# Kernel tuning notes

Measured on AMD Instinct MI355X. Metric: run time of the kernel, lower is better.

## Reference

```python
import jax, jax.numpy as jnp
import numpy as np

N_BINS = 10
A_CONST = 0.4
C_CONST = 500.0


def entropy(v, n=N_BINS):
    # Faithful to the torch loop: p_i = mean(v >= lo + i*s and v < lo + (i+1)*s),
    # entropy -= p*log(p) for p != 0. Vectorized over the n bins.
    v = v.reshape(-1)
    lo = v.min()
    hi = v.max()
    scale = (hi - lo) / n
    idx = jnp.arange(n, dtype=v.dtype)
    lower = lo + idx * scale                    # [n]
    upper = lower + scale                       # [n]
    mask = (v[None, :] >= lower[:, None]) & (v[None, :] < upper[:, None])  # [n, len(v)]
    p = mask.sum(axis=1).astype(v.dtype) / v.shape[0]
    safe_p = jnp.where(p > 0, p, 1.0)
    return -jnp.sum(jnp.where(p > 0, p * jnp.log(safe_p), 0.0))


def unite(p_i, p_j, w_assess, b_assess):
    # w_local = sigmoid(Linear(|p_i - p_j|)); w_global scalar from entropy gap.
    w_local = jax.nn.sigmoid(jnp.abs(p_i - p_j) @ w_assess.T + b_assess)
    w_global = A_CONST / jnp.pi * jnp.arctan(C_CONST * (entropy(p_i) - entropy(p_j))) + 0.5
    w = w_global * w_local + (1.0 - w_global)
    return p_i * w + p_j * (1.0 - w)


def setup_inputs() -> dict:
    key = jax.random.key(0)
    ks = jax.random.split(key, 11)
    B, S, H, L = 64, 512, 1024, 3
    s = 1.0 / np.sqrt(H)
    return {
        "x": jax.random.normal(ks[0], (B, S, H), jnp.float32),
        "base_dense_w": jax.random.normal(ks[1], (H, H), jnp.float32) * s,
        "base_dense_b": jax.random.normal(ks[2], (H,), jnp.float32) * s,
        "base_out_w": jax.random.normal(ks[3], (L, H), jnp.float32) * s,
        "base_out_b": jax.random.normal(ks[4], (L,), jnp.float32) * s,
        "graft_dense_w": jax.random.normal(ks[5], (H, H), jnp.float32) * s,
        "graft_out_w": jax.random.normal(ks[6], (L, H), jnp.float32) * s,
        "dense_assess_w": jax.random.normal(ks[7], (H, H), jnp.float32) * s,
        "dense_assess_b": jax.random.normal(ks[8], (H,), jnp.float32) * s,
        "out_assess_w": jax.random.normal(ks[9], (H, H), jnp.float32) * s,
        "out_assess_b": jax.random.normal(ks[10], (H,), jnp.float32) * s,
    }


def reference(x, base_dense_w, base_dense_b, base_out_w, base_out_b,
              graft_dense_w, graft_out_w,
              dense_assess_w, dense_assess_b, out_assess_w, out_assess_b):
    # roberta branch; dropout is identity (eval mode)
    h = x[:, 0, :]  # [B, H] CLS token
    # layer 0: dense
    pu0 = unite(base_dense_w, graft_dense_w, dense_assess_w, dense_assess_b)
    h = jnp.tanh(h @ pu0.T + base_dense_b)
    # layer 1: out_proj (final -> return)
    pu1 = unite(base_out_w, graft_out_w, out_assess_w, out_assess_b)
    return h @ pu1.T + base_out_b
```

## Files before the change

kernel.cpp:

```cpp
#include <hip/hip_runtime.h>
#include <hip/hip_bf16.h>
#include <math.h>


#define NBINS 10
typedef short bf8v __attribute__((ext_vector_type(8)));
typedef float f32x4 __attribute__((ext_vector_type(4)));
typedef unsigned long long u64;

#define AST(p, v) __hip_atomic_store((p), (v), __ATOMIC_RELAXED, __HIP_MEMORY_SCOPE_AGENT)
#define ALD(p)    __hip_atomic_load((p), __ATOMIC_RELAXED, __HIP_MEMORY_SCOPE_AGENT)

static __device__ __forceinline__ unsigned short f2bf(float f) {
    __hip_bfloat16 h = __float2bfloat16(f);
    return __builtin_bit_cast(unsigned short, h);
}

#define GL2LDS(gp, lp) __builtin_amdgcn_global_load_lds(                       \
    (__attribute__((address_space(1))) void*)(gp),                             \
    (__attribute__((address_space(3))) void*)(lp), 16, 0, 0)

static __device__ __forceinline__ void stage_slot(const unsigned short* __restrict__ src,
                                                  short* dst, int s, int row0, int k0) {
    int r = s >> 3, g = (s & 7) ^ (r & 7);
    GL2LDS(src + (size_t)(row0 + r) * 1024 + k0 + g * 8, dst + s * 8);
}
static __device__ __forceinline__ bf8v fr(const short* lds, int row, int G) {
    return ((const bf8v*)lds)[row * 8 + (G ^ (row & 7))];
}

static __device__ __forceinline__ float ent_bins(const unsigned* bins, float N) {
    float s = 0.0f;
    for (int b = 0; b < NBINS; b++) {
        float p = __fdiv_rn((float)ALD(&bins[b]), N);
        if (p > 0.0f) s += p * logf(p);
    }
    return -s;
}

__global__ __launch_bounds__(256) void k_prep(
    const float* __restrict__ x, const float* __restrict__ bdw, const float* __restrict__ bow,
    const float* __restrict__ gdw, const float* __restrict__ gow, const float* __restrict__ daw,
    const float* __restrict__ oaw, char* __restrict__ ws) {
    const int blk = blockIdx.x, t = threadIdx.x;
    const int lane = t & 63, wid = t >> 6;
    float* ws_f = (float*)ws;
    unsigned* ws_u = (unsigned*)ws;
    float* slots = ws_f + 1088;
    float* S1    = ws_f + 2112;
    unsigned short* Db  = (unsigned short*)(ws + 4456448);
    unsigned short* Wb  = (unsigned short*)(ws + 6553600);
    unsigned short* x0b = (unsigned short*)(ws + 8650752);
    __shared__ float sp[256];
    __shared__ float s_small[16];

    if (blk < 256) {
        float lo0 = INFINITY, hi0 = -INFINITY, lo1 = INFINITY, hi1 = -INFINITY;
        int fbase = blk * 1024 + t;
#pragma unroll
        for (int q = 0; q < 4; q++) {
            int idx = fbase + q * 256;
            float4 a = ((const float4*)bdw)[idx];
            float4 b = ((const float4*)gdw)[idx];
            float4 w = ((const float4*)daw)[idx];
            lo0 = fminf(lo0, fminf(fminf(a.x, a.y), fminf(a.z, a.w)));
            hi0 = fmaxf(hi0, fmaxf(fmaxf(a.x, a.y), fmaxf(a.z, a.w)));
            lo1 = fminf(lo1, fminf(fminf(b.x, b.y), fminf(b.z, b.w)));
            hi1 = fmaxf(hi1, fmaxf(fmaxf(b.x, b.y), fmaxf(b.z, b.w)));
            ushort4 d, ww;
            d.x = f2bf(fabsf(a.x - b.x)); d.y = f2bf(fabsf(a.y - b.y));
            d.z = f2bf(fabsf(a.z - b.z)); d.w = f2bf(fabsf(a.w - b.w));
            ww.x = f2bf(w.x); ww.y = f2bf(w.y); ww.z = f2bf(w.z); ww.w = f2bf(w.w);
            ((ushort4*)Db)[idx] = d;
            ((ushort4*)Wb)[idx] = ww;
        }
        for (int off = 32; off; off >>= 1) {
            lo0 = fminf(lo0, __shfl_down(lo0, off));
            hi0 = fmaxf(hi0, __shfl_down(hi0, off));
            lo1 = fminf(lo1, __shfl_down(lo1, off));
            hi1 = fmaxf(hi1, __shfl_down(hi1, off));
        }
        if (lane == 0) { s_small[wid] = lo0; s_small[4 + wid] = hi0; s_small[8 + wid] = lo1; s_small[12 + wid] = hi1; }
        __syncthreads();
        if (t == 0) {
            slots[blk]       = fminf(fminf(s_small[0], s_small[1]), fminf(s_small[2], s_small[3]));
            slots[256 + blk] = fmaxf(fmaxf(s_small[4], s_small[5]), fmaxf(s_small[6], s_small[7]));
            slots[512 + blk] = fminf(fminf(s_small[8], s_small[9]), fminf(s_small[10], s_small[11]));
            slots[768 + blk] = fmaxf(fmaxf(s_small[12], s_small[13]), fmaxf(s_small[14], s_small[15]));
        }
    } else {
        const int blk2 = blk - 256;
        {
            int d = t >> 4, kq = t & 15;
            if (d < 12) {
                int r = d >> 2, c = blk2 * 4 + (d & 3);
                const float4* bo4 = (const float4*)(bow + r * 1024);
                const float4* go4 = (const float4*)(gow + r * 1024);
                const float4* oa4 = (const float4*)(oaw + c * 1024);
                float s = 0.f;
#pragma unroll
                for (int k4 = kq * 16; k4 < kq * 16 + 16; ++k4) {
                    float4 bv = bo4[k4], gv = go4[k4], wv = oa4[k4];
                    s += fabsf(bv.x - gv.x) * wv.x + fabsf(bv.y - gv.y) * wv.y +
                         fabsf(bv.z - gv.z) * wv.z + fabsf(bv.w - gv.w) * wv.w;
                }
                sp[t] = s;
            }
            __syncthreads();
            if (t < 12) {
                float s = 0.f;
#pragma unroll
                for (int q = 0; q < 16; q++) s += sp[t * 16 + q];
                S1[(t >> 2) * 1024 + blk2 * 4 + (t & 3)] = s;
            }
        }
        if (blk == 256 || blk == 257) {
            const float* p = (blk == 256) ? bow : gow;
            float lo = INFINITY, hi = -INFINITY;
#pragma unroll
            for (int q = 0; q < 12; q++) { float v = p[q * 256 + t]; lo = fminf(lo, v); hi = fmaxf(hi, v); }
            for (int off = 32; off; off >>= 1) { lo = fminf(lo, __shfl_down(lo, off)); hi = fmaxf(hi, __shfl_down(hi, off)); }
            __syncthreads();
            if (lane == 0) { s_small[wid] = lo; s_small[4 + wid] = hi; }
            __syncthreads();
            if (t == 0) {
                ws_f[8 + 2 * (blk - 256)] = fminf(fminf(s_small[0], s_small[1]), fminf(s_small[2], s_small[3]));
                ws_f[9 + 2 * (blk - 256)] = fmaxf(fmaxf(s_small[4], s_small[5]), fmaxf(s_small[6], s_small[7]));
            }
        }
        if (blk == 258) {
#pragma unroll
            for (int q = 0; q < 4; q++) ws_u[64 + q * 256 + t] = 0u;
            if (t < 40) ws_u[16 + t] = 0u;
        }
        if (blk >= 260 && blk < 324) {
            int row = blk - 260;
            float4 v = ((const float4*)(x + (size_t)row * 524288))[t];
            ushort4 o; o.x = f2bf(v.x); o.y = f2bf(v.y); o.z = f2bf(v.z); o.w = f2bf(v.w);
            ((ushort4*)x0b)[row * 256 + t] = o;
        }
    }
}

__global__ __launch_bounds__(256) void k_main(
    const float* __restrict__ bdw, const float* __restrict__ gdw, const float* __restrict__ dab,
    const float* __restrict__ bow, const float* __restrict__ gow, const float* __restrict__ oab,
    const float* __restrict__ bdb, const float* __restrict__ bob,
    float* __restrict__ out, char* __restrict__ ws) {
    const int blk = blockIdx.x, t = threadIdx.x;
    const int lane = t & 63, wid = t >> 6;
    const int lr = lane & 15, k8 = lane >> 4;
    const int wr = wid >> 1, wc = wid & 1;

    float* ws_f = (float*)ws;
    unsigned* ws_u = (unsigned*)ws;
    unsigned* bins   = ws_u + 16;
    unsigned* flags1 = ws_u + 64;
    unsigned* flags2 = ws_u + 576;
    float* slots = ws_f + 1088;
    float* S1    = ws_f + 2112;
    float* pu1   = ws_f + 5248;
    float* part2 = ws_f + 16384;
    const unsigned short* Db  = (const unsigned short*)(ws + 4456448);
    const unsigned short* Wb  = (const unsigned short*)(ws + 6553600);
    const unsigned short* x0b = (const unsigned short*)(ws + 8650752);

    __shared__ short lds_a[2][2048];
    __shared__ short lds_b[2][4096];
    __shared__ short ldsT[32 * 72];
    __shared__ float ldsP[64 * 33];
    __shared__ float s_small[16];
    __shared__ unsigned s_hist[NBINS];
    __shared__ float s_wg[2];

    {
        int m, b0, nb;
        if (blk < 240)      { m = 0; b0 = blk;       nb = 240; }
        else if (blk < 480) { m = 1; b0 = blk - 240; nb = 240; }
        else if (blk < 496) { m = 2; b0 = blk - 480; nb = 16; }
        else                { m = 3; b0 = blk - 496; nb = 16; }
        const float* p = (m == 0) ? bdw : (m == 1) ? gdw : (m == 2) ? bow : gow;
        int n = (m < 2) ? 1048576 : 3072;
        float lo, hi;
        if (m < 2) {
            float l = slots[m * 512 + t];
            float h = slots[m * 512 + 256 + t];
            for (int off = 32; off; off >>= 1) { l = fminf(l, __shfl_down(l, off)); h = fmaxf(h, __shfl_down(h, off)); }
            if (lane == 0) { s_small[wid] = l; s_small[4 + wid] = h; }
            __syncthreads();
            lo = fminf(fminf(s_small[0], s_small[1]), fminf(s_small[2], s_small[3]));
            hi = fmaxf(fmaxf(s_small[4], s_small[5]), fmaxf(s_small[6], s_small[7]));
        } else {
            lo = ws_f[8 + 2 * (m - 2)];
            hi = ws_f[9 + 2 * (m - 2)];
        }
        float scale = __fdiv_rn(__fsub_rn(hi, lo), 10.0f);
        float lower[NBINS], upper[NBINS];
#pragma unroll
        for (int b = 0; b < NBINS; b++) {
            lower[b] = __fadd_rn(lo, __fmul_rn((float)b, scale));
            upper[b] = __fadd_rn(lower[b], scale);
        }
        unsigned cn[NBINS] = {};
#pragma unroll 4
        for (int i = b0 * 256 + t; i < n; i += nb * 256) {
            float v = p[i];
#pragma unroll
            for (int b = 0; b < NBINS; b++)
                if (v >= lower[b] && v < upper[b]) cn[b]++;
        }
        if (t < NBINS) s_hist[t] = 0;
        __syncthreads();
#pragma unroll
        for (int b = 0; b < NBINS; b++)
            if (cn[b]) atomicAdd(&s_hist[b], cn[b]);
        __syncthreads();
        if (t < NBINS && s_hist[t])
            __hip_atomic_fetch_add(&bins[m * NBINS + t], s_hist[t], __ATOMIC_RELAXED, __HIP_MEMORY_SCOPE_AGENT);
    }
    __syncthreads();
    if (t == 0) AST(&flags1[blk], 1u);

    const int c8 = blk & 7, rr = blk >> 3;
    const int bi = ((c8 >> 1) << 3) | (rr >> 3);
    const int bj = ((c8 & 1) << 3) | (rr & 7);
    f32x4 acc0 = {0.f, 0.f, 0.f, 0.f}, acc1 = {0.f, 0.f, 0.f, 0.f};
    {
        stage_slot(Db, lds_a[0], t, bi * 32, 0);
        stage_slot(Wb, lds_b[0], t, bj * 64, 0);
        stage_slot(Wb, lds_b[0], t + 256, bj * 64, 0);
        int cur = 0;
        for (int tt = 0; tt < 16; ++tt) {
            __syncthreads();
            if (tt + 1 < 16) {
                int k0 = (tt + 1) * 64;
                stage_slot(Db, lds_a[cur ^ 1], t, bi * 32, k0);
                stage_slot(Wb, lds_b[cur ^ 1], t, bj * 64, k0);
                stage_slot(Wb, lds_b[cur ^ 1], t + 256, bj * 64, k0);
            }
#pragma unroll
            for (int kk = 0; kk < 2; kk++) {
                bf8v a  = fr(lds_a[cur], wr * 16 + lr, kk * 4 + k8);
                bf8v b0 = fr(lds_b[cur], wc * 32 + lr, kk * 4 + k8);
                bf8v b1 = fr(lds_b[cur], wc * 32 + 16 + lr, kk * 4 + k8);
                acc0 = __builtin_amdgcn_mfma_f32_16x16x32_bf16(a, b0, acc0, 0, 0, 0);
                acc1 = __builtin_amdgcn_mfma_f32_16x16x32_bf16(a, b1, acc1, 0, 0, 0);
            }
            cur ^= 1;
        }
    }

    for (;;) {
        unsigned v0 = ALD(&flags1[t]);
        unsigned v1 = ALD(&flags1[t + 256]);
        if (__syncthreads_and((int)(v0 >= 1u && v1 >= 1u))) break;
        __builtin_amdgcn_s_sleep(1);
    }
    if (t == 0) {
        float e0 = ent_bins(&bins[0], 1048576.0f);
        float e1 = ent_bins(&bins[10], 1048576.0f);
        float e2 = ent_bins(&bins[20], 3072.0f);
        float e3 = ent_bins(&bins[30], 3072.0f);
        const float API = (float)(0.4 / M_PI);
        s_wg[0] = API * atanf(500.0f * (e0 - e1)) + 0.5f;
        s_wg[1] = API * atanf(500.0f * (e2 - e3)) + 0.5f;
    }
    __syncthreads();

    {
        float wg = s_wg[0];
#pragma unroll
        for (int j = 0; j < 2; j++) {
            f32x4 a = j ? acc1 : acc0;
#pragma unroll
            for (int r = 0; r < 4; r++) {
                int il = wr * 16 + k8 * 4 + r;
                int jl = wc * 32 + j * 16 + lr;
                int ig = bi * 32 + il, jg = bj * 64 + jl;
                float s = a[r] + dab[jg];
                float wl = 1.0f / (1.0f + expf(-s));
                float w = wg * wl + (1.0f - wg);
                float o = bdw[ig * 1024 + jg] * w + gdw[ig * 1024 + jg] * (1.0f - w);
                ldsT[il * 72 + jl] = (short)f2bf(o);
            }
        }
        __syncthreads();
        f32x4 ah0 = {0.f, 0.f, 0.f, 0.f}, ah1 = {0.f, 0.f, 0.f, 0.f};
#pragma unroll
        for (int ks = 0; ks < 2; ks++) {
            int cl = wc * 16 + lr;
            bf8v b = *(const bf8v*)&ldsT[cl * 72 + ks * 32 + k8 * 8];
            bf8v a0 = *(const bf8v*)&x0b[(wr * 32 + lr) * 1024 + bj * 64 + ks * 32 + k8 * 8];
            bf8v a1 = *(const bf8v*)&x0b[(wr * 32 + 16 + lr) * 1024 + bj * 64 + ks * 32 + k8 * 8];
            ah0 = __builtin_amdgcn_mfma_f32_16x16x32_bf16(a0, b, ah0, 0, 0, 0);
            ah1 = __builtin_amdgcn_mfma_f32_16x16x32_bf16(a1, b, ah1, 0, 0, 0);
        }
#pragma unroll
        for (int mi = 0; mi < 2; mi++) {
            f32x4 ah = mi ? ah1 : ah0;
#pragma unroll
            for (int r = 0; r < 4; r++)
                ldsP[(wr * 32 + mi * 16 + k8 * 4 + r) * 33 + wc * 16 + lr] = ah[r];
        }
        __syncthreads();
        {
            int m = t >> 2, c0 = (t & 3) * 8;
            const float* row = &ldsP[m * 33 + c0];
            float* gp = part2 + ((size_t)(bj * 64 + m) << 10) + bi * 32 + c0;
#pragma unroll
            for (int q = 0; q < 4; q++) {
                u64 u = ((u64)__float_as_uint(row[2 * q + 1]) << 32) | __float_as_uint(row[2 * q]);
                AST((u64*)(gp + 2 * q), u);
            }
        }
    }
    if (blk < 16 && t < 192) {
        int r = t >> 6, c = blk * 64 + (t & 63);
        float s1 = S1[r * 1024 + c];
        float wl = 1.0f / (1.0f + expf(-(s1 + oab[c])));
        float wg = s_wg[1];
        float w = wg * wl + (1.0f - wg);
        AST(&pu1[r * 1024 + c], bow[r * 1024 + c] * w + gow[r * 1024 + c] * (1.0f - w));
    }
    __syncthreads();
    if (t == 0) AST(&flags2[blk], 1u);

    if (blk < 64) {
        for (;;) {
            unsigned v0 = ALD(&flags2[t]);
            unsigned v1 = ALD(&flags2[t + 256]);
            if (__syncthreads_and((int)(v0 >= 1u && v1 >= 1u))) break;
            __builtin_amdgcn_s_sleep(1);
        }
        const int m = blk, c0 = t * 4;
        float s0 = 0, s1 = 0, s2 = 0, s3 = 0;
#pragma unroll
        for (int b = 0; b < 16; b++) {
            const float* pp = part2 + ((size_t)(b * 64 + m) << 10) + c0;
            u64 u0 = ALD((const u64*)pp);
            u64 u1 = ALD((const u64*)(pp + 2));
            s0 += __uint_as_float((unsigned)u0); s1 += __uint_as_float((unsigned)(u0 >> 32));
            s2 += __uint_as_float((unsigned)u1); s3 += __uint_as_float((unsigned)(u1 >> 32));
        }
        float h0 = tanhf(s0 + bdb[c0]);
        float h1 = tanhf(s1 + bdb[c0 + 1]);
        float h2 = tanhf(s2 + bdb[c0 + 2]);
        float h3 = tanhf(s3 + bdb[c0 + 3]);
        float p0, p1, p2;
        {
            u64 a0 = ALD((const u64*)(pu1 + c0)),        a1 = ALD((const u64*)(pu1 + c0 + 2));
            u64 b0 = ALD((const u64*)(pu1 + 1024 + c0)), b1 = ALD((const u64*)(pu1 + 1024 + c0 + 2));
            u64 d0 = ALD((const u64*)(pu1 + 2048 + c0)), d1 = ALD((const u64*)(pu1 + 2048 + c0 + 2));
            p0 = h0 * __uint_as_float((unsigned)a0) + h1 * __uint_as_float((unsigned)(a0 >> 32)) +
                 h2 * __uint_as_float((unsigned)a1) + h3 * __uint_as_float((unsigned)(a1 >> 32));
            p1 = h0 * __uint_as_float((unsigned)b0) + h1 * __uint_as_float((unsigned)(b0 >> 32)) +
                 h2 * __uint_as_float((unsigned)b1) + h3 * __uint_as_float((unsigned)(b1 >> 32));
            p2 = h0 * __uint_as_float((unsigned)d0) + h1 * __uint_as_float((unsigned)(d0 >> 32)) +
                 h2 * __uint_as_float((unsigned)d1) + h3 * __uint_as_float((unsigned)(d1 >> 32));
        }
        for (int off = 32; off; off >>= 1) {
            p0 += __shfl_down(p0, off);
            p1 += __shfl_down(p1, off);
            p2 += __shfl_down(p2, off);
        }
        if (lane == 0) { s_small[wid] = p0; s_small[4 + wid] = p1; s_small[8 + wid] = p2; }
        __syncthreads();
        if (t == 0) {
            out[m * 3 + 0] = s_small[0] + s_small[1] + s_small[2] + s_small[3] + bob[0];
            out[m * 3 + 1] = s_small[4] + s_small[5] + s_small[6] + s_small[7] + bob[1];
            out[m * 3 + 2] = s_small[8] + s_small[9] + s_small[10] + s_small[11] + bob[2];
        }
    }
}

extern "C" void kernel_launch(void* const* d_in, const int* in_sizes, int n_in,
                              void* d_out, int out_size, void* d_ws, size_t ws_size,
                              hipStream_t stream) {
    const float* x   = (const float*)d_in[0];
    const float* bdw = (const float*)d_in[1];
    const float* bdb = (const float*)d_in[2];
    const float* bow = (const float*)d_in[3];
    const float* bob = (const float*)d_in[4];
    const float* gdw = (const float*)d_in[5];
    const float* gow = (const float*)d_in[6];
    const float* daw = (const float*)d_in[7];
    const float* dab = (const float*)d_in[8];
    const float* oaw = (const float*)d_in[9];
    const float* oab = (const float*)d_in[10];
    float* out = (float*)d_out;
    char* ws = (char*)d_ws;

    k_prep<<<512, 256, 0, stream>>>(x, bdw, bow, gdw, gow, daw, oaw, ws);
    k_main<<<512, 256, 0, stream>>>(bdw, gdw, dab, bow, gow, oab, bdb, bob, out, ws);
}
```

Before: 57.12 us.

## Merge prep and main kernels into one persistent kernel with grid barrier

Folds the preprocessing kernel into the main kernel. All 512 blocks now share the prep work evenly and then wait at a flag-based grid barrier, and a single monotonically increasing flag array replaces the separate flag sets. Flag and bin zeroing moves to a hipMemsetAsync before the launch. This removes one kernel launch and the gap between kernels, at the cost of an extra grid-wide spin barrier and a memset call, and it relies on all 512 blocks being co-resident.

```diff
diff --git a/kernel.cpp b/kernel.cpp
--- a/kernel.cpp
+++ b/kernel.cpp
@@ -14,6 +14,9 @@
 static __device__ __forceinline__ unsigned short f2bf(float f) {
     __hip_bfloat16 h = __float2bfloat16(f);
     return __builtin_bit_cast(unsigned short, h);
+}
+static __device__ __forceinline__ u64 pack4(float a, float b, float c, float d) {
+    return (u64)f2bf(a) | ((u64)f2bf(b) << 16) | ((u64)f2bf(c) << 32) | ((u64)f2bf(d) << 48);
 }
 
 #define GL2LDS(gp, lp) __builtin_amdgcn_global_load_lds(                       \
@@ -38,28 +41,43 @@
     return -s;
 }
 
-__global__ __launch_bounds__(256) void k_prep(
-    const float* __restrict__ x, const float* __restrict__ bdw, const float* __restrict__ bow,
-    const float* __restrict__ gdw, const float* __restrict__ gow, const float* __restrict__ daw,
-    const float* __restrict__ oaw, char* __restrict__ ws) {
+__global__ __launch_bounds__(256) void k_mega(
+    const float* __restrict__ x, const float* __restrict__ bdw, const float* __restrict__ bdb,
+    const float* __restrict__ bow, const float* __restrict__ bob, const float* __restrict__ gdw,
+    const float* __restrict__ gow, const float* __restrict__ daw, const float* __restrict__ dab,
+    const float* __restrict__ oaw, const float* __restrict__ oab,
+    float* __restrict__ out, char* __restrict__ ws) {
     const int blk = blockIdx.x, t = threadIdx.x;
     const int lane = t & 63, wid = t >> 6;
+    const int lr = lane & 15, k8 = lane >> 4;
+    const int wr = wid >> 1, wc = wid & 1;
+
     float* ws_f = (float*)ws;
     unsigned* ws_u = (unsigned*)ws;
-    float* slots = ws_f + 1088;
-    float* S1    = ws_f + 2112;
+    unsigned* bins  = ws_u + 16;
+    unsigned* flags = ws_u + 64;
+    float* slots = ws_f + 2048;
+    float* S1    = ws_f + 4352;
+    float* pu1   = ws_f + 7680;
+    float* part2 = ws_f + 16384;
     unsigned short* Db  = (unsigned short*)(ws + 4456448);
     unsigned short* Wb  = (unsigned short*)(ws + 6553600);
     unsigned short* x0b = (unsigned short*)(ws + 8650752);
-    __shared__ float sp[256];
+
+    __shared__ short lds_a[2][2048];
+    __shared__ short lds_b[2][4096];
+    __shared__ short ldsT[32 * 72];
+    __shared__ float ldsP[64 * 33];
     __shared__ float s_small[16];
-
-    if (blk < 256) {
+    __shared__ unsigned s_hist[NBINS];
+    __shared__ float s_wg[2];
+
+    {
         float lo0 = INFINITY, hi0 = -INFINITY, lo1 = INFINITY, hi1 = -INFINITY;
-        int fbase = blk * 1024 + t;
-#pragma unroll
-        for (int q = 0; q < 4; q++) {
-            int idx = fbase + q * 256;
+        int base = blk * 512;
+#pragma unroll
+        for (int q = 0; q < 2; q++) {
+            int idx = base + q * 256 + t;
             float4 a = ((const float4*)bdw)[idx];
             float4 b = ((const float4*)gdw)[idx];
             float4 w = ((const float4*)daw)[idx];
@@ -67,12 +85,31 @@
             hi0 = fmaxf(hi0, fmaxf(fmaxf(a.x, a.y), fmaxf(a.z, a.w)));
             lo1 = fminf(lo1, fminf(fminf(b.x, b.y), fminf(b.z, b.w)));
             hi1 = fmaxf(hi1, fmaxf(fmaxf(b.x, b.y), fmaxf(b.z, b.w)));
-            ushort4 d, ww;
-            d.x = f2bf(fabsf(a.x - b.x)); d.y = f2bf(fabsf(a.y - b.y));
-            d.z = f2bf(fabsf(a.z - b.z)); d.w = f2bf(fabsf(a.w - b.w));
-            ww.x = f2bf(w.x); ww.y = f2bf(w.y); ww.z = f2bf(w.z); ww.w = f2bf(w.w);
-            ((ushort4*)Db)[idx] = d;
-            ((ushort4*)Wb)[idx] = ww;
+            AST((u64*)Db + idx, pack4(fabsf(a.x - b.x), fabsf(a.y - b.y),
+                                      fabsf(a.z - b.z), fabsf(a.w - b.w)));
+            AST((u64*)Wb + idx, pack4(w.x, w.y, w.z, w.w));
+        }
+        {
+            int d = t >> 5, kq = t & 31;
+            if (d < 6) {
+                int g = blk * 6 + d, r = g >> 10, c = g & 1023;
+                const float4* bo4 = (const float4*)(bow + r * 1024);
+                const float4* go4 = (const float4*)(gow + r * 1024);
+                const float4* oa4 = (const float4*)(oaw + c * 1024);
+                float s = 0.f;
+#pragma unroll
+                for (int k4 = kq * 8; k4 < kq * 8 + 8; ++k4) {
+                    float4 bv = bo4[k4], gv = go4[k4], wv = oa4[k4];
+                    s += fabsf(bv.x - gv.x) * wv.x + fabsf(bv.y - gv.y) * wv.y +
+                         fabsf(bv.z - gv.z) * wv.z + fabsf(bv.w - gv.w) * wv.w;
+                }
+                for (int off = 16; off; off >>= 1) s += __shfl_xor(s, off);
+                if (kq == 0) AST(&S1[g], s);
+            }
+        }
+        if (blk < 64) {
+            float4 v = ((const float4*)(x + (size_t)blk * 524288))[t];
+            AST((u64*)x0b + blk * 256 + t, pack4(v.x, v.y, v.z, v.w));
         }
         for (int off = 32; off; off >>= 1) {
             lo0 = fminf(lo0, __shfl_down(lo0, off));
@@ -83,39 +120,13 @@
         if (lane == 0) { s_small[wid] = lo0; s_small[4 + wid] = hi0; s_small[8 + wid] = lo1; s_small[12 + wid] = hi1; }
         __syncthreads();
         if (t == 0) {
-            slots[blk]       = fminf(fminf(s_small[0], s_small[1]), fminf(s_small[2], s_small[3]));
-            slots[256 + blk] = fmaxf(fmaxf(s_small[4], s_small[5]), fmaxf(s_small[6], s_small[7]));
-            slots[512 + blk] = fminf(fminf(s_small[8], s_small[9]), fminf(s_small[10], s_small[11]));
-            slots[768 + blk] = fmaxf(fmaxf(s_small[12], s_small[13]), fmaxf(s_small[14], s_small[15]));
-        }
-    } else {
-        const int blk2 = blk - 256;
-        {
-            int d = t >> 4, kq = t & 15;
-            if (d < 12) {
-                int r = d >> 2, c = blk2 * 4 + (d & 3);
-                const float4* bo4 = (const float4*)(bow + r * 1024);
-                const float4* go4 = (const float4*)(gow + r * 1024);
-                const float4* oa4 = (const float4*)(oaw + c * 1024);
-                float s = 0.f;
-#pragma unroll
-                for (int k4 = kq * 16; k4 < kq * 16 + 16; ++k4) {
-                    float4 bv = bo4[k4], gv = go4[k4], wv = oa4[k4];
-                    s += fabsf(bv.x - gv.x) * wv.x + fabsf(bv.y - gv.y) * wv.y +
-                         fabsf(bv.z - gv.z) * wv.z + fabsf(bv.w - gv.w) * wv.w;
-                }
-                sp[t] = s;
-            }
-            __syncthreads();
-            if (t < 12) {
-                float s = 0.f;
-#pragma unroll
-                for (int q = 0; q < 16; q++) s += sp[t * 16 + q];
-                S1[(t >> 2) * 1024 + blk2 * 4 + (t & 3)] = s;
-            }
-        }
-        if (blk == 256 || blk == 257) {
-            const float* p = (blk == 256) ? bow : gow;
+            AST(&slots[blk],        fminf(fminf(s_small[0], s_small[1]), fminf(s_small[2], s_small[3])));
+            AST(&slots[512 + blk],  fmaxf(fmaxf(s_small[4], s_small[5]), fmaxf(s_small[6], s_small[7])));
+            AST(&slots[1024 + blk], fminf(fminf(s_small[8], s_small[9]), fminf(s_small[10], s_small[11])));
+            AST(&slots[1536 + blk], fmaxf(fmaxf(s_small[12], s_small[13]), fmaxf(s_small[14], s_small[15])));
+        }
+        if (blk == 510 || blk == 511) {
+            const float* p = (blk == 510) ? bow : gow;
             float lo = INFINITY, hi = -INFINITY;
 #pragma unroll
             for (int q = 0; q < 12; q++) { float v = p[q * 256 + t]; lo = fminf(lo, v); hi = fmaxf(hi, v); }
@@ -124,54 +135,19 @@
             if (lane == 0) { s_small[wid] = lo; s_small[4 + wid] = hi; }
             __syncthreads();
             if (t == 0) {
-                ws_f[8 + 2 * (blk - 256)] = fminf(fminf(s_small[0], s_small[1]), fminf(s_small[2], s_small[3]));
-                ws_f[9 + 2 * (blk - 256)] = fmaxf(fmaxf(s_small[4], s_small[5]), fmaxf(s_small[6], s_small[7]));
-            }
-        }
-        if (blk == 258) {
-#pragma unroll
-            for (int q = 0; q < 4; q++) ws_u[64 + q * 256 + t] = 0u;
-            if (t < 40) ws_u[16 + t] = 0u;
-        }
-        if (blk >= 260 && blk < 324) {
-            int row = blk - 260;
-            float4 v = ((const float4*)(x + (size_t)row * 524288))[t];
-            ushort4 o; o.x = f2bf(v.x); o.y = f2bf(v.y); o.z = f2bf(v.z); o.w = f2bf(v.w);
-            ((ushort4*)x0b)[row * 256 + t] = o;
-        }
-    }
-}
-
-__global__ __launch_bounds__(256) void k_main(
-    const float* __restrict__ bdw, const float* __restrict__ gdw, const float* __restrict__ dab,
-    const float* __restrict__ bow, const float* __restrict__ gow, const float* __restrict__ oab,
-    const float* __restrict__ bdb, const float* __restrict__ bob,
-    float* __restrict__ out, char* __restrict__ ws) {
-    const int blk = blockIdx.x, t = threadIdx.x;
-    const int lane = t & 63, wid = t >> 6;
-    const int lr = lane & 15, k8 = lane >> 4;
-    const int wr = wid >> 1, wc = wid & 1;
-
-    float* ws_f = (float*)ws;
-    unsigned* ws_u = (unsigned*)ws;
-    unsigned* bins   = ws_u + 16;
-    unsigned* flags1 = ws_u + 64;
-    unsigned* flags2 = ws_u + 576;
-    float* slots = ws_f + 1088;
-    float* S1    = ws_f + 2112;
-    float* pu1   = ws_f + 5248;
-    float* part2 = ws_f + 16384;
-    const unsigned short* Db  = (const unsigned short*)(ws + 4456448);
-    const unsigned short* Wb  = (const unsigned short*)(ws + 6553600);
-    const unsigned short* x0b = (const unsigned short*)(ws + 8650752);
-
-    __shared__ short lds_a[2][2048];
-    __shared__ short lds_b[2][4096];
-    __shared__ short ldsT[32 * 72];
-    __shared__ float ldsP[64 * 33];
-    __shared__ float s_small[16];
-    __shared__ unsigned s_hist[NBINS];
-    __shared__ float s_wg[2];
+                AST(&ws_f[1088 + 2 * (blk - 510)], fminf(fminf(s_small[0], s_small[1]), fminf(s_small[2], s_small[3])));
+                AST(&ws_f[1089 + 2 * (blk - 510)], fmaxf(fmaxf(s_small[4], s_small[5]), fmaxf(s_small[6], s_small[7])));
+            }
+        }
+    }
+    __syncthreads();
+    if (t == 0) AST(&flags[blk], 1u);
+    for (;;) {
+        unsigned v0 = ALD(&flags[t]);
+        unsigned v1 = ALD(&flags[t + 256]);
+        if (__syncthreads_and((int)(v0 >= 1u && v1 >= 1u))) break;
+        __builtin_amdgcn_s_sleep(1);
+    }
 
     {
         int m, b0, nb;
@@ -183,16 +159,16 @@
         int n = (m < 2) ? 1048576 : 3072;
         float lo, hi;
         if (m < 2) {
-            float l = slots[m * 512 + t];
-            float h = slots[m * 512 + 256 + t];
+            float l = fminf(ALD(&slots[m * 1024 + t]),       ALD(&slots[m * 1024 + 256 + t]));
+            float h = fmaxf(ALD(&slots[m * 1024 + 512 + t]), ALD(&slots[m * 1024 + 768 + t]));
             for (int off = 32; off; off >>= 1) { l = fminf(l, __shfl_down(l, off)); h = fmaxf(h, __shfl_down(h, off)); }
             if (lane == 0) { s_small[wid] = l; s_small[4 + wid] = h; }
             __syncthreads();
             lo = fminf(fminf(s_small[0], s_small[1]), fminf(s_small[2], s_small[3]));
             hi = fmaxf(fmaxf(s_small[4], s_small[5]), fmaxf(s_small[6], s_small[7]));
         } else {
-            lo = ws_f[8 + 2 * (m - 2)];
-            hi = ws_f[9 + 2 * (m - 2)];
+            lo = ALD(&ws_f[1088 + 2 * (m - 2)]);
+            hi = ALD(&ws_f[1089 + 2 * (m - 2)]);
         }
         float scale = __fdiv_rn(__fsub_rn(hi, lo), 10.0f);
         float lower[NBINS], upper[NBINS];
@@ -219,7 +195,7 @@
             __hip_atomic_fetch_add(&bins[m * NBINS + t], s_hist[t], __ATOMIC_RELAXED, __HIP_MEMORY_SCOPE_AGENT);
     }
     __syncthreads();
-    if (t == 0) AST(&flags1[blk], 1u);
+    if (t == 0) AST(&flags[blk], 2u);
 
     const int c8 = blk & 7, rr = blk >> 3;
     const int bi = ((c8 >> 1) << 3) | (rr >> 3);
@@ -251,9 +227,9 @@
     }
 
     for (;;) {
-        unsigned v0 = ALD(&flags1[t]);
-        unsigned v1 = ALD(&flags1[t + 256]);
-        if (__syncthreads_and((int)(v0 >= 1u && v1 >= 1u))) break;
+        unsigned v0 = ALD(&flags[t]);
+        unsigned v1 = ALD(&flags[t + 256]);
+        if (__syncthreads_and((int)(v0 >= 2u && v1 >= 2u))) break;
         __builtin_amdgcn_s_sleep(1);
     }
     if (t == 0) {
@@ -316,20 +292,20 @@
     }
     if (blk < 16 && t < 192) {
         int r = t >> 6, c = blk * 64 + (t & 63);
-        float s1 = S1[r * 1024 + c];
+        float s1 = ALD(&S1[r * 1024 + c]);
         float wl = 1.0f / (1.0f + expf(-(s1 + oab[c])));
         float wg = s_wg[1];
         float w = wg * wl + (1.0f - wg);
         AST(&pu1[r * 1024 + c], bow[r * 1024 + c] * w + gow[r * 1024 + c] * (1.0f - w));
     }
     __syncthreads();
-    if (t == 0) AST(&flags2[blk], 1u);
+    if (t == 0) AST(&flags[blk], 3u);
 
     if (blk < 64) {
         for (;;) {
-            unsigned v0 = ALD(&flags2[t]);
-            unsigned v1 = ALD(&flags2[t + 256]);
-            if (__syncthreads_and((int)(v0 >= 1u && v1 >= 1u))) break;
+            unsigned v0 = ALD(&flags[t]);
+            unsigned v1 = ALD(&flags[t + 256]);
+            if (__syncthreads_and((int)(v0 >= 3u && v1 >= 3u))) break;
             __builtin_amdgcn_s_sleep(1);
         }
         const int m = blk, c0 = t * 4;
@@ -390,6 +366,7 @@
     float* out = (float*)d_out;
     char* ws = (char*)d_ws;
 
-    k_prep<<<512, 256, 0, stream>>>(x, bdw, bow, gdw, gow, daw, oaw, ws);
-    k_main<<<512, 256, 0, stream>>>(bdw, gdw, dab, bow, gow, oab, bdb, bob, out, ws);
-}
+    hipMemsetAsync(d_ws, 0, 2560, stream);
+    k_mega<<<512, 256, 0, stream>>>(x, bdw, bdb, bow, bob, gdw, gow, daw, dab,
+                                    oaw, oab, out, ws);
+}
```

Result: slower. 69.39 us (+21.5%).
